# Performance work log

Measured on AMD Instinct MI355X. Metric: run time of the kernel, lower is better.

Reference implementation:

```python
import jax, jax.numpy as jnp
import numpy as np

B, L = 16, 512
H_RNN = 300
EMB, POSD, POSTD = 300, 30, 30
IN_DIM = EMB + POSD + POSTD  # 360
HEADS, MEM = 8, 300
DM = 2 * MEM                 # 600
DK = DM // HEADS             # 75
VOCAB, NPOS, NPOST = 30000, 50, 120
ALPHA, BETA = 0.8, 0.9
N_ASP = 3


def _lstm_dir(x, w_ih, w_hh, b_ih, b_hh, reverse):
    # x: [B,L,D] -> [B,L,H]; PyTorch gate order i,f,g,o
    xs = jnp.swapaxes(x, 0, 1)
    if reverse:
        xs = xs[::-1]
    pre = xs @ w_ih.T + (b_ih + b_hh)  # [L,B,4H]
    Bn = x.shape[0]
    H = w_hh.shape[1]

    def step(carry, p):
        h, c = carry
        g = p + h @ w_hh.T
        i, f, gg, o = jnp.split(g, 4, axis=-1)
        c = jax.nn.sigmoid(f) * c + jax.nn.sigmoid(i) * jnp.tanh(gg)
        h = jax.nn.sigmoid(o) * jnp.tanh(c)
        return (h, c), h

    init = (jnp.zeros((Bn, H), x.dtype), jnp.zeros((Bn, H), x.dtype))
    _, hs = jax.lax.scan(step, init, pre)
    if reverse:
        hs = hs[::-1]
    return jnp.swapaxes(hs, 0, 1)


def _forward(tok, pos, post, asp_mask, adj_reshape, emb_w, pos_w, post_w,
             w_ih_f, w_hh_f, b_ih_f, b_hh_f, w_ih_b, w_hh_b, b_ih_b, b_hh_b,
             wq, bq, wk, bk, wd, bd, weight_m, bias_m,
             wa0, ba0, wa1, ba1, ws0, bs0, ws1, bs1, affine1, affine2):
    Bn, Ln = tok.shape
    embs = jnp.concatenate([emb_w[tok], pos_w[pos], post_w[post]], -1)  # [B,L,360]
    hf = _lstm_dir(embs, w_ih_f, w_hh_f, b_ih_f, b_hh_f, False)
    hb = _lstm_dir(embs, w_ih_b, w_hh_b, b_ih_b, b_hh_b, True)
    gcn_inputs = jnp.concatenate([hf, hb], -1)  # [B,L,600]
    tok_mask = tok != 0
    aspect_outs = gcn_inputs * asp_mask[:, :, None]

    q = (gcn_inputs @ wq.T + bq).reshape(Bn, Ln, HEADS, DK).transpose(0, 2, 1, 3)
    k = (gcn_inputs @ wk.T + bk).reshape(Bn, Ln, HEADS, DK).transpose(0, 2, 1, 3)
    aspd = aspect_outs @ wd.T + bd  # [B,L,DK], shared across heads
    t = jnp.einsum('bld,hde->bhle', aspd, weight_m)
    asps = jnp.tanh(jnp.einsum('bhle,bhme->bhlm', t, k) + bias_m[0])  # [B,h,L,L]

    # fusion branch: vectorized equivalent of the ragged row/col scatter-average.
    # Original loop: for each aspect idx (ascending), row idx <- avg vec, then col idx <- avg vec.
    avg = asps.sum(-2) / Ln  # [B,h,L]
    amask = asp_mask > 0
    r = jnp.arange(Ln)[:, None]
    c = jnp.arange(Ln)[None, :]
    rA = amask[:, None, :, None]
    cA = amask[:, None, None, :]
    col_wins = cA & (~rA | (c > r))
    aspect_scores = jnp.where(col_wins, avg[:, :, :, None],
                              jnp.where(rA, avg[:, :, None, :], asps))

    scores = jnp.einsum('bhld,bhmd->bhlm', q, k) / np.float32(np.sqrt(DK))
    scores = jnp.where(tok_mask[:, None, None, :], scores, -1e9)
    s_attn = jax.nn.softmax(scores, -1)

    asavg = aspect_scores.mean(1)  # [B,L,L]
    adj_s = s_attn.mean(1)
    eye = jnp.eye(Ln, dtype=adj_s.dtype)
    adj_s = (adj_s * (1.0 - eye) + eye) * tok_mask[:, :, None].astype(adj_s.dtype)

    adj_r = jnp.where(asavg > BETA, 1.0, jnp.exp(ALPHA * adj_reshape))
    adj_ag = adj_r * asavg

    denom_s = adj_s.sum(2, keepdims=True) + 1.0
    denom_ag = adj_ag.sum(2, keepdims=True) + 1.0
    out_ag = out_s = gcn_inputs
    for wa_, ba_, ws_, bs_ in ((wa0, ba0, ws0, bs0), (wa1, ba1, ws1, bs1)):
        g_ag = jax.nn.relu(((adj_ag @ out_ag) @ wa_.T + ba_) / denom_ag)
        g_s = jax.nn.relu(((adj_s @ out_s) @ ws_.T + bs_) / denom_s)
        A1 = jax.nn.softmax(jnp.einsum('bld,de,bme->blm', g_ag, affine1, g_s), -1)
        A2 = jax.nn.softmax(jnp.einsum('bld,de,bme->blm', g_s, affine2, g_ag), -1)
        out_ag, out_s = A1 @ g_s, A2 @ g_ag
    return jnp.concatenate([out_ag, out_s], -1)  # [B,L,600]


def setup_inputs():
    key = jax.random.key(0)
    ks = jax.random.split(key, 40)

    def nrm(i, shape):
        return jax.random.normal(ks[i], shape, jnp.float32) * 0.02

    tok = jax.random.randint(ks[0], (B, L), 1, VOCAB, jnp.int32)
    pos = jax.random.randint(ks[1], (B, L), 0, NPOS, jnp.int32)
    post = jax.random.randint(ks[2], (B, L), 0, NPOST, jnp.int32)
    asp_mask = jnp.zeros((B, L), jnp.float32).at[:, 3:3 + N_ASP].set(1.0)
    l = jnp.full((B,), L, jnp.int32)
    adj_reshape = jax.random.uniform(ks[3], (B, L, L), jnp.float32)
    return dict(
        tok=tok, pos=pos, post=post, asp_mask=asp_mask, l=l, adj_reshape=adj_reshape,
        emb_w=nrm(4, (VOCAB, EMB)), pos_w=nrm(5, (NPOS, POSD)), post_w=nrm(6, (NPOST, POSTD)),
        w_ih_f=nrm(7, (4 * H_RNN, IN_DIM)), w_hh_f=nrm(8, (4 * H_RNN, H_RNN)),
        b_ih_f=nrm(9, (4 * H_RNN,)), b_hh_f=nrm(10, (4 * H_RNN,)),
        w_ih_b=nrm(11, (4 * H_RNN, IN_DIM)), w_hh_b=nrm(12, (4 * H_RNN, H_RNN)),
        b_ih_b=nrm(13, (4 * H_RNN,)), b_hh_b=nrm(14, (4 * H_RNN,)),
        wq=nrm(15, (DM, DM)), bq=nrm(16, (DM,)), wk=nrm(17, (DM, DM)), bk=nrm(18, (DM,)),
        wd=nrm(19, (DK, DM)), bd=nrm(20, (DK,)),
        weight_m=nrm(21, (HEADS, DK, DK)), bias_m=nrm(22, (1,)),
        wa0=nrm(23, (MEM, DM)), ba0=nrm(24, (MEM,)), wa1=nrm(25, (MEM, MEM)), ba1=nrm(26, (MEM,)),
        ws0=nrm(27, (MEM, DM)), bs0=nrm(28, (MEM,)), ws1=nrm(29, (MEM, MEM)), bs1=nrm(30, (MEM,)),
        affine1=nrm(31, (MEM, MEM)), affine2=nrm(32, (MEM, MEM)))


def reference(tok, pos, post, asp_mask, l, adj_reshape, emb_w, pos_w, post_w,
              w_ih_f, w_hh_f, b_ih_f, b_hh_f, w_ih_b, w_hh_b, b_ih_b, b_hh_b,
              wq, bq, wk, bk, wd, bd, weight_m, bias_m,
              wa0, ba0, wa1, ba1, ws0, bs0, ws1, bs1, affine1, affine2):
    # l is all-maxlen by construction (no padding); pack/pad is identity.
    return _forward(tok, pos, post, asp_mask, adj_reshape, emb_w, pos_w, post_w,
                    w_ih_f, w_hh_f, b_ih_f, b_hh_f, w_ih_b, w_hh_b, b_ih_b, b_hh_b,
                    wq, bq, wk, bk, wd, bd, weight_m, bias_m,
                    wa0, ba0, wa1, ba1, ws0, bs0, ws1, bs1, affine1, affine2)
```

## Files before the change

kernel.cpp:

```cpp
#include <hip/hip_runtime.h>
#include <hip/hip_bf16.h>

typedef __hip_bfloat16 bf16;
typedef __attribute__((ext_vector_type(4))) short short4v;
typedef __attribute__((ext_vector_type(8))) short short8v;
typedef __attribute__((ext_vector_type(4))) float f32x4;
typedef unsigned long long u64;

#define B_   16
#define L_   512
#define HR   300
#define DM_  600
#define DK_  75
#define MAXA 8
#define NCH  38

__global__ __launch_bounds__(256) void k_embed(
    const int* __restrict__ tok, const int* __restrict__ pos, const int* __restrict__ post,
    const float* __restrict__ emb_w, const float* __restrict__ pos_w, const float* __restrict__ post_w,
    float* __restrict__ embs)
{
  int idx = blockIdx.x * 256 + threadIdx.x;
  if (idx >= L_ * B_ * 360) return;
  int d = idx % 360;
  int seq = idx / 360;
  int b = seq & 15, t = seq >> 4;
  int si = b * L_ + t;
  float v;
  if (d < 300)       v = emb_w[(long)tok[si] * 300 + d];
  else if (d < 330)  v = pos_w[pos[si] * 30 + (d - 300)];
  else               v = post_w[post[si] * 30 + (d - 330)];
  embs[idx] = v;
}

__global__ __launch_bounds__(256) void k_stage(
    const float* __restrict__ wq, const float* __restrict__ wk,
    const float* __restrict__ bq, const float* __restrict__ bk,
    const float* __restrict__ wihf, const float* __restrict__ wihb,
    const float* __restrict__ aff1, const float* __restrict__ aff2,
    const float* __restrict__ ws0, const float* __restrict__ wa0,
    const float* __restrict__ ws1, const float* __restrict__ wa1,
    const float* __restrict__ bs0, const float* __restrict__ ba0,
    const float* __restrict__ bs1, const float* __restrict__ ba1,
    float* __restrict__ wqk, float* __restrict__ bqk,
    float* __restrict__ wih, float* __restrict__ aff,
    float* __restrict__ wsa, float* __restrict__ bsa)
{
  int i = blockIdx.x * 256 + threadIdx.x;
  if (i < 360000) wqk[i] = wq[i];
  else if (i < 720000) wqk[i] = wk[i - 360000];
  else if (i < 720600) bqk[i - 720000] = bq[i - 720000];
  else if (i < 721200) bqk[i - 720000] = bk[i - 720600];
  else if (i < 1153200) wih[i - 721200] = wihf[i - 721200];
  else if (i < 1585200) wih[i - 721200] = wihb[i - 1153200];
  else if (i < 1675200) aff[i - 1585200] = aff1[i - 1585200];
  else if (i < 1765200) aff[i - 1585200] = aff2[i - 1675200];
  else if (i < 1945200) wsa[i - 1765200] = ws0[i - 1765200];
  else if (i < 2125200) wsa[i - 1765200] = wa0[i - 1945200];
  else if (i < 2215200) wsa[i - 1765200] = ws1[i - 2125200];
  else if (i < 2305200) wsa[i - 1765200] = wa1[i - 2215200];
  else if (i < 2305500) bsa[i - 2305200] = bs0[i - 2305200];
  else if (i < 2305800) bsa[i - 2305200] = ba0[i - 2305500];
  else if (i < 2306100) bsa[i - 2305200] = bs1[i - 2305800];
  else if (i < 2306400) bsa[i - 2305200] = ba1[i - 2306100];
}

__device__ inline short2 splitf(float x) {
  unsigned u = __float_as_uint(x);
  unsigned hb = u & 0xffff0000u;
  float r = x - __uint_as_float(hb);
  unsigned lb = __float_as_uint(r);
  short2 out;
  out.x = (short)(hb >> 16);
  out.y = (short)(lb >> 16);
  return out;
}

__device__ inline short8v ld_frag(const short* p) {
  short4v a = *reinterpret_cast<const short4v*>(p);
  short4v b = *reinterpret_cast<const short4v*>(p + 16);
  short8v r;
  r[0]=a[0]; r[1]=a[1]; r[2]=a[2]; r[3]=a[3];
  r[4]=b[0]; r[5]=b[1]; r[6]=b[2]; r[7]=b[3];
  return r;
}

#define LDA_ 36

template<bool NT>
__global__ __launch_bounds__(256) void k_mgemm(
    const float* __restrict__ A, int lda, long sA1, long sA2,
    const float* __restrict__ Bm, int ldb, long sB1, long sB2,
    float* __restrict__ C, bf16* __restrict__ Cbf, int ldc, long sC1, long sC2,
    const float* __restrict__ bias, long sBias,
    const float* __restrict__ rowdiv,
    float alpha, int relu, int M, int N, int K, int nb2)
{
  __shared__ short Ah[128 * LDA_], Al[128 * LDA_], Bh[64 * LDA_], Bl[64 * LDA_];
  const int tid = threadIdx.x;
  const int w = tid >> 6, l = tid & 63;
  const int z = blockIdx.z;
  const int b1 = z / nb2, b2 = z - b1 * nb2;
  const float* Ab = A + b1 * sA1 + b2 * sA2;
  const float* Bb = Bm + b1 * sB1 + b2 * sB2;
  const int row0 = blockIdx.y * 128, col0 = blockIdx.x * 64;

  f32x4 acc[2][4];
#pragma unroll
  for (int f = 0; f < 2; ++f)
#pragma unroll
    for (int c = 0; c < 4; ++c) acc[f][c] = (f32x4){0.f, 0.f, 0.f, 0.f};

  const int lrow = l & 15, lk = (l >> 4) * 4;

  for (int k0 = 0; k0 < K; k0 += 32) {
#pragma unroll
    for (int j = 0; j < 4; ++j) {
      int slot = j * 256 + tid;
      int r = slot >> 3, kq = slot & 7;
      int gr = row0 + r, gk = k0 + kq * 4;
      float v[4] = {0.f, 0.f, 0.f, 0.f};
      if (gr < M) {
        if (gk + 3 < K) {
          float4 t = *reinterpret_cast<const float4*>(Ab + (long)gr * lda + gk);
          v[0] = t.x; v[1] = t.y; v[2] = t.z; v[3] = t.w;
        } else {
#pragma unroll
          for (int q = 0; q < 4; ++q) if (gk + q < K) v[q] = Ab[(long)gr * lda + gk + q];
        }
      }
      short4v hv, lv;
#pragma unroll
      for (int q = 0; q < 4; ++q) {
        short2 t2 = splitf(v[q]);
        hv[q] = t2.x; lv[q] = t2.y;
      }
      *reinterpret_cast<short4v*>(&Ah[r * LDA_ + kq * 4]) = hv;
      *reinterpret_cast<short4v*>(&Al[r * LDA_ + kq * 4]) = lv;
    }
    if (NT) {
#pragma unroll
      for (int j = 0; j < 2; ++j) {
        int slot = j * 256 + tid;
        int r = slot >> 3, kq = slot & 7;
        int gc = col0 + r, gk = k0 + kq * 4;
        float v[4] = {0.f, 0.f, 0.f, 0.f};
        if (gc < N) {
          if (gk + 3 < K) {
            float4 t = *reinterpret_cast<const float4*>(Bb + (long)gc * ldb + gk);
            v[0] = t.x; v[1] = t.y; v[2] = t.z; v[3] = t.w;
          } else {
#pragma unroll
            for (int q = 0; q < 4; ++q) if (gk + q < K) v[q] = Bb[(long)gc * ldb + gk + q];
          }
        }
        short4v hv, lv;
#pragma unroll
        for (int q = 0; q < 4; ++q) {
          short2 t2 = splitf(v[q]);
          hv[q] = t2.x; lv[q] = t2.y;
        }
        *reinterpret_cast<short4v*>(&Bh[r * LDA_ + kq * 4]) = hv;
        *reinterpret_cast<short4v*>(&Bl[r * LDA_ + kq * 4]) = lv;
      }
    } else {
#pragma unroll
      for (int j = 0; j < 2; ++j) {
        int slot = j * 256 + tid;
        int kk = slot >> 4, nq = slot & 15;
        int gk = k0 + kk, gn = col0 + nq * 4;
        float v[4] = {0.f, 0.f, 0.f, 0.f};
        if (gk < K) {
          if (gn + 3 < N) {
            float4 t = *reinterpret_cast<const float4*>(Bb + (long)gk * ldb + gn);
            v[0] = t.x; v[1] = t.y; v[2] = t.z; v[3] = t.w;
          } else {
#pragma unroll
            for (int q = 0; q < 4; ++q) if (gn + q < N) v[q] = Bb[(long)gk * ldb + gn + q];
          }
        }
#pragma unroll
        for (int q = 0; q < 4; ++q) {
          short2 t2 = splitf(v[q]);
          Bh[(nq * 4 + q) * LDA_ + kk] = t2.x;
          Bl[(nq * 4 + q) * LDA_ + kk] = t2.y;
        }
      }
    }
    __syncthreads();

    short8v ah[2], al[2];
#pragma unroll
    for (int f = 0; f < 2; ++f) {
      int ar = w * 32 + f * 16 + lrow;
      ah[f] = ld_frag(&Ah[ar * LDA_ + lk]);
      al[f] = ld_frag(&Al[ar * LDA_ + lk]);
    }
#pragma unroll
    for (int c = 0; c < 4; ++c) {
      short8v bh = ld_frag(&Bh[(c * 16 + lrow) * LDA_ + lk]);
      short8v bl = ld_frag(&Bl[(c * 16 + lrow) * LDA_ + lk]);
#pragma unroll
      for (int f = 0; f < 2; ++f) {
        acc[f][c] = __builtin_amdgcn_mfma_f32_16x16x32_bf16(ah[f], bh, acc[f][c], 0, 0, 0);
        acc[f][c] = __builtin_amdgcn_mfma_f32_16x16x32_bf16(ah[f], bl, acc[f][c], 0, 0, 0);
        acc[f][c] = __builtin_amdgcn_mfma_f32_16x16x32_bf16(al[f], bh, acc[f][c], 0, 0, 0);
      }
    }
    __syncthreads();
  }

  float* Cb = C ? C + b1 * sC1 + b2 * sC2 : (float*)0;
  bf16*  Cf = Cbf ? Cbf + b1 * sC1 + b2 * sC2 : (bf16*)0;
#pragma unroll
  for (int f = 0; f < 2; ++f)
#pragma unroll
  for (int c = 0; c < 4; ++c) {
    int cc = col0 + c * 16 + lrow;
    if (cc >= N) continue;
#pragma unroll
    for (int reg = 0; reg < 4; ++reg) {
      int r = row0 + w * 32 + f * 16 + (l >> 4) * 4 + reg;
      if (r >= M) continue;
      float v = acc[f][c][reg] * alpha;
      if (bias) v += bias[b1 * sBias + cc];
      if (rowdiv) v /= rowdiv[(long)z * M + r];
      if (relu) v = fmaxf(v, 0.f);
      if (Cf) Cf[(long)r * ldc + cc] = __float2bfloat16(v);
      else    Cb[(long)r * ldc + cc] = v;
    }
  }
}

__global__ __launch_bounds__(512, 1) void k_lstm(
    const float* __restrict__ preT_f, const float* __restrict__ preT_b,
    const float* __restrict__ whh_f, const float* __restrict__ whh_b,
    const float* __restrict__ bih_f, const float* __restrict__ bhh_f,
    const float* __restrict__ bih_b, const float* __restrict__ bhh_b,
    float* __restrict__ gcn, u64* __restrict__ hg)
{
  const int tid = threadIdx.x;
  const int dir = blockIdx.x / NCH;
  const int blk = blockIdx.x - dir * NCH;
  const int u0 = blk * 8;
  const int uc = min(8, HR - u0);
  const float* pre = dir ? preT_b : preT_f;
  const float* whh = dir ? whh_b : whh_f;
  const float* bih = dir ? bih_b : bih_f;
  const float* bhh = dir ? bhh_b : bhh_f;
  u64* hgd = hg + dir * 2400;

  __shared__ float4 h5[1200];
  __shared__ float part[32 * 545 + 64];
  __shared__ float g_lds[512];
  float* h5f = reinterpret_cast<float*>(h5);

  const int kc = tid >> 4;
  const int rq = tid & 15;
  const int kl = (kc < 12) ? 10 : 9;
  const int k0 = kc * 9 + min(kc, 12);

  float wreg[2][10];
#pragma unroll
  for (int i = 0; i < 2; ++i) {
    int lr = rq * 2 + i;
    int gate = lr >> 3, unit = lr & 7;
    bool valid = unit < uc;
    int growc = gate * HR + u0 + min(unit, uc - 1);
#pragma unroll
    for (int kk = 0; kk < 10; ++kk) {
      int k = min(k0 + kk, 299);
      float wv = whh[(long)growc * HR + k];
      wreg[i][kk] = (valid && kk < kl) ? wv : 0.f;
    }
  }

  const int lr0 = tid >> 4;
  const int b0 = tid & 15;
  const int gate0 = lr0 >> 3, unit0 = lr0 & 7;
  const int grow0 = gate0 * HR + u0 + min(unit0, uc - 1);
  const float breg = bih[grow0] + bhh[grow0];
  const float* prebase = pre + (long)grow0 * 8192;

  const int au = tid >> 3, abp = tid & 7;
  float c_reg0 = 0.f, c_reg1 = 0.f;

  const int own_lo = u0 * 8, own_hi = (u0 + uc) * 8;

#pragma unroll 1
  for (int s = 0; s < L_; ++s) {
    const int tf = dir ? (L_ - 1 - s) : s;

    float p0 = prebase[tf * 16 + b0];

    if (s > 0) {
      u64* srcb = hgd + (s & 1) * 4800;
      const u64 tag = (u64)s;
      u64 vals[5];
      int idxs[5];
#pragma unroll
      for (int j = 0; j < 5; ++j) {
        int idx = tid + j * 512;
        bool act = (idx < 2400) && (idx < own_lo || idx >= own_hi);
        idxs[j] = act ? idx : -1;
        vals[j] = act ? __hip_atomic_load(&srcb[idx], __ATOMIC_RELAXED, __HIP_MEMORY_SCOPE_AGENT)
                      : (tag << 32);
      }
      for (;;) {
        bool ok = true;
#pragma unroll
        for (int j = 0; j < 5; ++j)
          if ((vals[j] >> 32) != tag) ok = false;
        if (ok) break;
#pragma unroll
        for (int j = 0; j < 5; ++j)
          if ((vals[j] >> 32) != tag)
            vals[j] = __hip_atomic_load(&srcb[idxs[j]], __ATOMIC_RELAXED, __HIP_MEMORY_SCOPE_AGENT);
      }
#pragma unroll
      for (int j = 0; j < 5; ++j) {
        int idx = idxs[j];
        if (idx >= 0) {
          unsigned lo = (unsigned)(vals[j] & 0xffffffffu);
          unsigned short be = (unsigned short)(lo & 0xffffu);
          unsigned short bo = (unsigned short)(lo >> 16);
          bf16 he = *reinterpret_cast<bf16*>(&be);
          bf16 ho = *reinterpret_cast<bf16*>(&bo);
          int u = idx >> 3, bp = idx & 7;
          h5f[u * 16 + bp * 2]     = __bfloat162float(he);
          h5f[u * 16 + bp * 2 + 1] = __bfloat162float(ho);
        }
      }
    }
    __syncthreads();

    if (s > 0) {
      float4 acc[2][4];
#pragma unroll
      for (int i = 0; i < 2; ++i)
#pragma unroll
        for (int q = 0; q < 4; ++q) acc[i][q] = make_float4(0.f, 0.f, 0.f, 0.f);
#pragma unroll
      for (int kk = 0; kk < 10; ++kk) {
        if (kk < kl) {
          int k = k0 + kk;
          float4 hb0 = h5[k * 4 + 0];
          float4 hb1 = h5[k * 4 + 1];
          float4 hb2 = h5[k * 4 + 2];
          float4 hb3 = h5[k * 4 + 3];
#pragma unroll
          for (int i = 0; i < 2; ++i) {
            float w = wreg[i][kk];
            acc[i][0].x = fmaf(w, hb0.x, acc[i][0].x); acc[i][0].y = fmaf(w, hb0.y, acc[i][0].y);
            acc[i][0].z = fmaf(w, hb0.z, acc[i][0].z); acc[i][0].w = fmaf(w, hb0.w, acc[i][0].w);
            acc[i][1].x = fmaf(w, hb1.x, acc[i][1].x); acc[i][1].y = fmaf(w, hb1.y, acc[i][1].y);
            acc[i][1].z = fmaf(w, hb1.z, acc[i][1].z); acc[i][1].w = fmaf(w, hb1.w, acc[i][1].w);
            acc[i][2].x = fmaf(w, hb2.x, acc[i][2].x); acc[i][2].y = fmaf(w, hb2.y, acc[i][2].y);
            acc[i][2].z = fmaf(w, hb2.z, acc[i][2].z); acc[i][2].w = fmaf(w, hb2.w, acc[i][2].w);
            acc[i][3].x = fmaf(w, hb3.x, acc[i][3].x); acc[i][3].y = fmaf(w, hb3.y, acc[i][3].y);
            acc[i][3].z = fmaf(w, hb3.z, acc[i][3].z); acc[i][3].w = fmaf(w, hb3.w, acc[i][3].w);
          }
        }
      }
#pragma unroll
      for (int i = 0; i < 2; ++i) {
        int lr = rq * 2 + i;
        float* pb = part + kc * 545 + lr * 17;
#pragma unroll
        for (int q = 0; q < 4; ++q) {
          pb[q * 4 + 0] = acc[i][q].x; pb[q * 4 + 1] = acc[i][q].y;
          pb[q * 4 + 2] = acc[i][q].z; pb[q * 4 + 3] = acc[i][q].w;
        }
      }
    }
    __syncthreads();

    float g0 = p0 + breg;
    if (s > 0) {
      const float* pb = part + lr0 * 17 + b0;
#pragma unroll
      for (int q = 0; q < 32; ++q) g0 += pb[q * 545];
    }
    g_lds[tid] = g0;
    __syncthreads();

    if (tid < 64 && au < uc) {
      int be = abp * 2, bo = abp * 2 + 1;
      float gi0 = g_lds[(0 * 8 + au) * 16 + be];
      float gf0 = g_lds[(1 * 8 + au) * 16 + be];
      float gg0 = g_lds[(2 * 8 + au) * 16 + be];
      float go0 = g_lds[(3 * 8 + au) * 16 + be];
      float gi1 = g_lds[(0 * 8 + au) * 16 + bo];
      float gf1 = g_lds[(1 * 8 + au) * 16 + bo];
      float gg1 = g_lds[(2 * 8 + au) * 16 + bo];
      float go1 = g_lds[(3 * 8 + au) * 16 + bo];
      float si0 = 1.f / (1.f + __expf(-gi0));
      float sf0 = 1.f / (1.f + __expf(-gf0));
      float so0 = 1.f / (1.f + __expf(-go0));
      float tg0 = tanhf(gg0);
      float si1 = 1.f / (1.f + __expf(-gi1));
      float sf1 = 1.f / (1.f + __expf(-gf1));
      float so1 = 1.f / (1.f + __expf(-go1));
      float tg1 = tanhf(gg1);
      c_reg0 = sf0 * c_reg0 + si0 * tg0;
      c_reg1 = sf1 * c_reg1 + si1 * tg1;
      float h0 = so0 * tanhf(c_reg0);
      float h1 = so1 * tanhf(c_reg1);
      h5f[(u0 + au) * 16 + be] = h0;
      h5f[(u0 + au) * 16 + bo] = h1;
      bf16 hbe = __float2bfloat16(h0);
      bf16 hbo = __float2bfloat16(h1);
      unsigned bitse = *reinterpret_cast<unsigned short*>(&hbe);
      unsigned bitso = *reinterpret_cast<unsigned short*>(&hbo);
      u64 val = ((u64)(s + 1) << 32) | ((u64)bitso << 16) | (u64)bitse;
      __hip_atomic_store(&hgd[((s + 1) & 1) * 4800 + (u0 + au) * 8 + abp], val,
                         __ATOMIC_RELAXED, __HIP_MEMORY_SCOPE_AGENT);
      gcn[((long)be * L_ + tf) * DM_ + dir * HR + u0 + au] = h0;
      gcn[((long)bo * L_ + tf) * DM_ + dir * HR + u0 + au] = h1;
    }
  }
}

__global__ void k_asplist(const float* __restrict__ asp_mask, int* __restrict__ apos, int* __restrict__ acnt)
{
  int b = threadIdx.x;
  if (b >= B_) return;
  int c = 0;
  for (int l = 0; l < L_; ++l)
    if (asp_mask[b * L_ + l] > 0.f) { if (c < MAXA) apos[b * MAXA + c] = l; ++c; }
  acnt[b] = (c < MAXA) ? c : MAXA;
}

__global__ void k_t0(const float* __restrict__ bd, const float* __restrict__ wm, float* __restrict__ t0)
{
  int i = blockIdx.x * 256 + threadIdx.x;
  if (i >= 8 * DK_) return;
  int h = i / DK_, e = i % DK_;
  float s = 0.f;
  for (int d = 0; d < DK_; ++d) s += bd[d] * wm[(h * DK_ + d) * DK_ + e];
  t0[i] = s;
}

__global__ void k_aspd(const float* __restrict__ gcn, const float* __restrict__ asp_mask,
                       const int* __restrict__ apos, const int* __restrict__ acnt,
                       const float* __restrict__ wd, const float* __restrict__ bd, float* __restrict__ aspd)
{
  int i = blockIdx.x * 256 + threadIdx.x;
  if (i >= B_ * MAXA * DK_) return;
  int d = i % DK_;
  int ba = i / DK_;
  int a = ba % MAXA, b = ba / MAXA;
  if (a >= acnt[b]) { aspd[i] = 0.f; return; }
  int p = apos[b * MAXA + a];
  float mv = asp_mask[b * L_ + p];
  const float* row = gcn + ((long)b * L_ + p) * DM_;
  float s = 0.f;
  for (int k = 0; k < DM_; ++k) s += row[k] * wd[d * DM_ + k];
  aspd[i] = s * mv + bd[d];
}

__global__ void k_tasp(const float* __restrict__ aspd, const int* __restrict__ acnt,
                       const float* __restrict__ wm, float* __restrict__ tasp)
{
  int i = blockIdx.x * 256 + threadIdx.x;
  if (i >= B_ * 8 * MAXA * DK_) return;
  int e = i % DK_;
  int t3 = i / DK_;
  int a = t3 % MAXA;
  int t4 = t3 / MAXA;
  int h = t4 % 8, b = t4 / 8;
  if (a >= acnt[b]) { tasp[i] = 0.f; return; }
  const float* ar = aspd + (b * MAXA + a) * DK_;
  float s = 0.f;
  for (int d = 0; d < DK_; ++d) s += ar[d] * wm[(h * DK_ + d) * DK_ + e];
  tasp[i] = s;
}

__global__ void k_avg(const float* __restrict__ k_lin, const float* __restrict__ t0,
                      const float* __restrict__ tasp, const int* __restrict__ acnt,
                      const float* __restrict__ bias_m, float* __restrict__ s0, float* __restrict__ avg)
{
  int i = blockIdx.x * 256 + threadIdx.x;
  if (i >= B_ * 8 * L_) return;
  int m = i % L_;
  int bh = i / L_;
  int h = bh % 8, b = bh / 8;
  const float* kr = k_lin + ((long)b * L_ + m) * DM_ + h * DK_;
  float bm = bias_m[0];
  const float* t0r = t0 + h * DK_;
  float d0 = 0.f;
  for (int e = 0; e < DK_; ++e) d0 += t0r[e] * kr[e];
  float sv = tanhf(d0 + bm);
  int cnt = acnt[b];
  float acc = (float)(L_ - cnt) * sv;
  for (int a = 0; a < cnt; ++a) {
    const float* tr = tasp + (((b * 8 + h) * MAXA) + a) * DK_;
    float dd = 0.f;
    for (int e = 0; e < DK_; ++e) dd += tr[e] * kr[e];
    acc += tanhf(dd + bm);
  }
  s0[i] = sv;
  avg[i] = acc * (1.f / (float)L_);
}

__global__ void k_bar(const float* __restrict__ s0, const float* __restrict__ avg,
                      float* __restrict__ s0bar, float* __restrict__ avbar)
{
  int i = blockIdx.x * 256 + threadIdx.x;
  if (i >= B_ * L_) return;
  int m = i % L_, b = i / L_;
  float sa = 0.f, aa = 0.f;
  for (int h = 0; h < 8; ++h) { sa += s0[(b * 8 + h) * L_ + m]; aa += avg[(b * 8 + h) * L_ + m]; }
  s0bar[i] = sa * 0.125f;
  avbar[i] = aa * 0.125f;
}

__global__ __launch_bounds__(256) void k_adjag(
    const float* __restrict__ asp_mask, const float* __restrict__ adjr,
    const float* __restrict__ s0bar, const float* __restrict__ avbar,
    float* __restrict__ adjag, float* __restrict__ denag)
{
  int bl = blockIdx.x;
  int b = bl >> 9, l = bl & 511;
  bool rA = asp_mask[b * L_ + l] > 0.f;
  float avl = avbar[b * L_ + l];
  float lsum = 0.f;
  for (int q = 0; q < 2; ++q) {
    int m = threadIdx.x + q * 256;
    bool cA = asp_mask[b * L_ + m] > 0.f;
    float asv;
    if (cA && (!rA || m > l)) asv = avl;
    else if (rA)              asv = avbar[b * L_ + m];
    else                      asv = s0bar[b * L_ + m];
    float r = (asv > 0.9f) ? 1.f : __expf(0.8f * adjr[((long)b * L_ + l) * L_ + m]);
    float v = r * asv;
    adjag[((long)b * L_ + l) * L_ + m] = v;
    lsum += v;
  }
  __shared__ float red[256];
  red[threadIdx.x] = lsum;
  __syncthreads();
  for (int st = 128; st > 0; st >>= 1) {
    if (threadIdx.x < st) red[threadIdx.x] += red[threadIdx.x + st];
    __syncthreads();
  }
  if (threadIdx.x == 0) denag[bl] = red[0] + 1.f;
}

__global__ __launch_bounds__(256) void k_adjs2(
    const bf16* __restrict__ sc, const int* __restrict__ tok,
    float* __restrict__ adjs, float* __restrict__ dens)
{
  int bl = blockIdx.x;
  int b = bl >> 9, l = bl & 511;
  int tid = threadIdx.x;
  __shared__ float srow[8][512];
  __shared__ float stats[16];
  __shared__ float red[256];

  int t0v = tok[b * L_ + tid], t1v = tok[b * L_ + tid + 256];
#pragma unroll
  for (int h = 0; h < 8; ++h) {
    const bf16* p = sc + ((long)((b * 8 + h) * L_) + l) * L_;
    float v0 = __bfloat162float(p[tid]);
    float v1 = __bfloat162float(p[tid + 256]);
    srow[h][tid]       = (t0v != 0) ? v0 : -1e9f;
    srow[h][tid + 256] = (t1v != 0) ? v1 : -1e9f;
  }
  __syncthreads();

  int wv = tid >> 6, lane = tid & 63;
#pragma unroll
  for (int hh = 0; hh < 2; ++hh) {
    int h = wv * 2 + hh;
    float vv[8];
#pragma unroll
    for (int i = 0; i < 8; ++i) vv[i] = srow[h][lane + i * 64];
    float m = vv[0];
#pragma unroll
    for (int i = 1; i < 8; ++i) m = fmaxf(m, vv[i]);
    for (int off = 32; off > 0; off >>= 1) m = fmaxf(m, __shfl_xor(m, off));
    float s = 0.f;
#pragma unroll
    for (int i = 0; i < 8; ++i) s += __expf(vv[i] - m);
    for (int off = 32; off > 0; off >>= 1) s += __shfl_xor(s, off);
    if (lane == 0) { stats[h] = m; stats[8 + h] = 1.f / s; }
  }
  __syncthreads();

  float acc0 = 0.f, acc1 = 0.f;
#pragma unroll
  for (int h = 0; h < 8; ++h) {
    float m = stats[h], inv = stats[8 + h];
    acc0 += __expf(srow[h][tid] - m) * inv;
    acc1 += __expf(srow[h][tid + 256] - m) * inv;
  }
  float rmask = (tok[b * L_ + l] != 0) ? 1.f : 0.f;
  float lsum = 0.f;
  {
    int m = tid;
    float v = acc0 * 0.125f;
    v = (m == l) ? 1.f : v;
    v *= rmask;
    adjs[(long)bl * L_ + m] = v;
    lsum += v;
  }
  {
    int m = tid + 256;
    float v = acc1 * 0.125f;
    v = (m == l) ? 1.f : v;
    v *= rmask;
    adjs[(long)bl * L_ + m] = v;
    lsum += v;
  }
  red[tid] = lsum;
  __syncthreads();
  for (int st = 128; st > 0; st >>= 1) {
    if (tid < st) red[tid] += red[tid + st];
    __syncthreads();
  }
  if (tid == 0) dens[bl] = red[0] + 1.f;
}

__global__ __launch_bounds__(256) void k_softmax(float* __restrict__ X)
{
  long row = blockIdx.x;
  float* p = X + row * L_;
  int tid = threadIdx.x;
  float a = p[tid], b = p[tid + 256];
  __shared__ float red[256];
  red[tid] = fmaxf(a, b);
  __syncthreads();
  for (int st = 128; st > 0; st >>= 1) {
    if (tid < st) red[tid] = fmaxf(red[tid], red[tid + st]);
    __syncthreads();
  }
  float mxv = red[0];
  __syncthreads();
  float ea = __expf(a - mxv), eb = __expf(b - mxv);
  red[tid] = ea + eb;
  __syncthreads();
  for (int st = 128; st > 0; st >>= 1) {
    if (tid < st) red[tid] += red[tid + st];
    __syncthreads();
  }
  float inv = 1.f / red[0];
  p[tid] = ea * inv;
  p[tid + 256] = eb * inv;
}

static void gemm(hipStream_t st, bool nt,
                 const float* A, int lda, long sA1, long sA2,
                 const float* Bm, int ldb, long sB1, long sB2,
                 float* C, bf16* Cbf, int ldc, long sC1, long sC2,
                 const float* bias, long sBias, const float* rowdiv,
                 float alpha, int relu, int M, int N, int K, int nb1, int nb2)
{
  dim3 g((N + 63) / 64, (M + 127) / 128, nb1 * nb2);
  if (nt)
    k_mgemm<true><<<g, 256, 0, st>>>(A, lda, sA1, sA2, Bm, ldb, sB1, sB2, C, Cbf, ldc, sC1, sC2,
                                     bias, sBias, rowdiv, alpha, relu, M, N, K, nb2);
  else
    k_mgemm<false><<<g, 256, 0, st>>>(A, lda, sA1, sA2, Bm, ldb, sB1, sB2, C, Cbf, ldc, sC1, sC2,
                                      bias, sBias, rowdiv, alpha, relu, M, N, K, nb2);
}

extern "C" void kernel_launch(void* const* d_in, const int* in_sizes, int n_in,
                              void* d_out, int out_size, void* d_ws, size_t ws_size,
                              hipStream_t stream)
{
  const int*   tok     = (const int*)d_in[0];
  const int*   pos     = (const int*)d_in[1];
  const int*   post    = (const int*)d_in[2];
  const float* asp_mask= (const float*)d_in[3];
  const float* adjr    = (const float*)d_in[5];
  const float* emb_w   = (const float*)d_in[6];
  const float* pos_w   = (const float*)d_in[7];
  const float* post_w  = (const float*)d_in[8];
  const float* w_ih_f  = (const float*)d_in[9];
  const float* w_hh_f  = (const float*)d_in[10];
  const float* b_ih_f  = (const float*)d_in[11];
  const float* b_hh_f  = (const float*)d_in[12];
  const float* w_ih_b  = (const float*)d_in[13];
  const float* w_hh_b  = (const float*)d_in[14];
  const float* b_ih_b  = (const float*)d_in[15];
  const float* b_hh_b  = (const float*)d_in[16];
  const float* wq      = (const float*)d_in[17];
  const float* bq      = (const float*)d_in[18];
  const float* wk      = (const float*)d_in[19];
  const float* bk      = (const float*)d_in[20];
  const float* wd      = (const float*)d_in[21];
  const float* bd      = (const float*)d_in[22];
  const float* wm      = (const float*)d_in[23];
  const float* bias_m  = (const float*)d_in[24];
  const float* wa0     = (const float*)d_in[25];
  const float* ba0     = (const float*)d_in[26];
  const float* wa1     = (const float*)d_in[27];
  const float* ba1     = (const float*)d_in[28];
  const float* ws0     = (const float*)d_in[29];
  const float* bs0     = (const float*)d_in[30];
  const float* ws1     = (const float*)d_in[31];
  const float* bs1     = (const float*)d_in[32];
  const float* aff1    = (const float*)d_in[33];
  const float* aff2    = (const float*)d_in[34];
  float* out = (float*)d_out;
  float* W = (float*)d_ws;

  size_t off = 0;
  auto alloc = [&](size_t n) { size_t o = off; off += (n + 63) & ~(size_t)63; return o; };
  size_t o_gcn   = alloc((size_t)8192 * DM_);
  size_t o_q     = alloc((size_t)8192 * DM_);
  size_t o_k     = alloc((size_t)8192 * DM_);
  size_t o_adjs  = alloc((size_t)B_ * L_ * L_);
  size_t o_adjag = alloc((size_t)B_ * L_ * L_);
  size_t o_dens  = alloc(8192);
  size_t o_denag = alloc(8192);
  size_t o_t0    = alloc(600);
  size_t o_apos  = alloc(B_ * MAXA);
  size_t o_acnt  = alloc(64);
  size_t o_aspd  = alloc(B_ * MAXA * DK_);
  size_t o_tasp  = alloc(B_ * 8 * MAXA * DK_);
  size_t o_s0    = alloc(B_ * 8 * L_);
  size_t o_avg   = alloc(B_ * 8 * L_);
  size_t o_s0bar = alloc(B_ * L_);
  size_t o_avbar = alloc(B_ * L_);
  size_t o_hg    = alloc(2 * 2 * 4800);
  size_t o_wqk   = alloc(720000);
  size_t o_bqk   = alloc(1200);
  size_t o_wih   = alloc(864000);
  size_t o_aff   = alloc(180000);
  size_t o_wsa   = alloc(540000);
  size_t o_bsa   = alloc(1200);
  size_t o_oag1  = alloc((size_t)8192 * 300);
  size_t o_os1   = alloc((size_t)8192 * 300);
  size_t o_big   = alloc(23134300);
  size_t o_embs = o_big;
  size_t o_pref = o_big + 2949120;
  size_t o_preb = o_pref + 9830400;
  size_t o_sc   = o_big;
  size_t o_tmp  = o_big;
  size_t o_gag  = o_big + 4915200;
  size_t o_gs   = o_gag + 2457600;
  size_t o_h1   = o_gs  + 2457600;
  size_t o_a1m  = o_h1  + 4915200;
  size_t o_a2m  = o_a1m + 4194304;

  if (ws_size < off * sizeof(float)) {
    (void)hipMemsetAsync(d_out, 0x7F, (size_t)out_size * sizeof(float), stream);
    return;
  }

  k_stage<<<(2306400 + 255) / 256, 256, 0, stream>>>(
      wq, wk, bq, bk, w_ih_f, w_ih_b, aff1, aff2,
      ws0, wa0, ws1, wa1, bs0, ba0, bs1, ba1,
      W + o_wqk, W + o_bqk, W + o_wih, W + o_aff, W + o_wsa, W + o_bsa);

  k_embed<<<(L_ * B_ * 360 + 255) / 256, 256, 0, stream>>>(tok, pos, post, emb_w, pos_w, post_w, W + o_embs);

  gemm(stream, true, W + o_wih, 360, 432000, 0, W + o_embs, 360, 0, 0,
       W + o_pref, nullptr, 8192, 9830400, 0, nullptr, 0, nullptr, 1.f, 0, 1200, 8192, 360, 2, 1);

  k_lstm<<<2 * NCH, 512, 0, stream>>>(W + o_pref, W + o_preb, w_hh_f, w_hh_b,
                                      b_ih_f, b_hh_f, b_ih_b, b_hh_b,
                                      W + o_gcn, (u64*)(W + o_hg));

  gemm(stream, true, W + o_gcn, DM_, 0, 0, W + o_wqk, DM_, 360000, 0,
       W + o_q, nullptr, DM_, (long)(o_k - o_q), 0, W + o_bqk, 600, nullptr,
       1.f, 0, 8192, DM_, DM_, 2, 1);

  k_asplist<<<1, 64, 0, stream>>>(asp_mask, (int*)(W + o_apos), (int*)(W + o_acnt));
  k_t0<<<(600 + 255) / 256, 256, 0, stream>>>(bd, wm, W + o_t0);
  k_aspd<<<(B_ * MAXA * DK_ + 255) / 256, 256, 0, stream>>>(W + o_gcn, asp_mask,
      (const int*)(W + o_apos), (const int*)(W + o_acnt), wd, bd, W + o_aspd);
  k_tasp<<<(B_ * 8 * MAXA * DK_ + 255) / 256, 256, 0, stream>>>(W + o_aspd,
      (const int*)(W + o_acnt), wm, W + o_tasp);
  k_avg<<<(B_ * 8 * L_ + 255) / 256, 256, 0, stream>>>(W + o_k, W + o_t0, W + o_tasp,
      (const int*)(W + o_acnt), bias_m, W + o_s0, W + o_avg);
  k_bar<<<(B_ * L_ + 255) / 256, 256, 0, stream>>>(W + o_s0, W + o_avg, W + o_s0bar, W + o_avbar);

  gemm(stream, true, W + o_q, DM_, (long)L_ * DM_, DK_, W + o_k, DM_, (long)L_ * DM_, DK_,
       nullptr, (bf16*)(W + o_sc), L_, (long)8 * L_ * L_, (long)L_ * L_,
       nullptr, 0, nullptr, 0.1154700538f, 0, L_, L_, DK_, B_, 8);
  k_adjs2<<<B_ * L_, 256, 0, stream>>>((const bf16*)(W + o_sc), tok, W + o_adjs, W + o_dens);
  k_adjag<<<B_ * L_, 256, 0, stream>>>(asp_mask, adjr, W + o_s0bar, W + o_avbar,
                                       W + o_adjag, W + o_denag);

  const float* inBase;
  long inStride;
  const long tmpStride = (long)o_tmp - (long)o_a1m;
  int D = DM_;
  for (int layer = 0; layer < 2; ++layer) {
    if (layer == 0) { inBase = W + o_gcn; inStride = 0; }
    else            { inBase = W + o_os1; inStride = (long)o_oag1 - (long)o_os1; }
    gemm(stream, false,
         W + o_adjs, L_, (long)o_adjag - (long)o_adjs, (long)L_ * L_,
         inBase, D, inStride, (long)L_ * D,
         W + o_a1m, nullptr, D, tmpStride, (long)L_ * D,
         nullptr, 0, nullptr, 1.f, 0, L_, D, L_, 2, B_);
    gemm(stream, true,
         W + o_a1m, D, tmpStride, 0,
         W + o_wsa + (layer ? 360000 : 0), D, (layer ? 90000 : 180000), 0,
         W + o_gs, nullptr, 300, (long)o_gag - (long)o_gs, 0,
         W + o_bsa + (layer ? 600 : 0), 300, W + o_dens,
         1.f, 1, 8192, 300, D, 2, 1);
    gemm(stream, false, W + o_gag, 300, (long)(o_gs - o_gag), 0, W + o_aff, 300, 90000, 0,
         W + o_h1, nullptr, 300, 2457600, 0, nullptr, 0, nullptr, 1.f, 0, 8192, 300, 300, 2, 1);
    gemm(stream, true, W + o_h1, 300, 2457600, (long)L_ * 300,
         W + o_gs, 300, (long)o_gag - (long)o_gs, (long)L_ * 300,
         W + o_a1m, nullptr, L_, 4194304, (long)L_ * L_,
         nullptr, 0, nullptr, 1.f, 0, L_, L_, 300, 2, B_);
    k_softmax<<<2 * B_ * L_, 256, 0, stream>>>(W + o_a1m);
    float* dstC; int ldcO; long sC1o, sC2o;
    if (layer == 0) { dstC = W + o_oag1; ldcO = 300; sC1o = (long)(o_os1 - o_oag1); sC2o = (long)L_ * 300; }
    else            { dstC = out;        ldcO = 600; sC1o = 300;                    sC2o = (long)L_ * 600; }
    gemm(stream, false, W + o_a1m, L_, 4194304, (long)L_ * L_,
         W + o_gs, 300, (long)o_gag - (long)o_gs, (long)L_ * 300,
         dstC, nullptr, ldcO, sC1o, sC2o,
         nullptr, 0, nullptr, 1.f, 0, L_, 300, L_, 2, B_);
    D = 300;
  }
}
```

Before: 2.779 ms.

## Split LSTM recurrence across 75 blocks per direction with 4 units each

```diff
diff --git a/kernel.cpp b/kernel.cpp
--- a/kernel.cpp
+++ b/kernel.cpp
@@ -13,7 +13,7 @@
 #define DM_  600
 #define DK_  75
 #define MAXA 8
-#define NCH  38
+#define NCH  75
 
 __global__ __launch_bounds__(256) void k_embed(
     const int* __restrict__ tok, const int* __restrict__ pos, const int* __restrict__ post,
@@ -242,8 +242,7 @@
   const int tid = threadIdx.x;
   const int dir = blockIdx.x / NCH;
   const int blk = blockIdx.x - dir * NCH;
-  const int u0 = blk * 8;
-  const int uc = min(8, HR - u0);
+  const int u0 = blk * 4;
   const float* pre = dir ? preT_b : preT_f;
   const float* whh = dir ? whh_b : whh_f;
   const float* bih = dir ? bih_b : bih_f;
@@ -251,8 +250,8 @@
   u64* hgd = hg + dir * 2400;
 
   __shared__ float4 h5[1200];
-  __shared__ float part[32 * 545 + 64];
-  __shared__ float g_lds[512];
+  __shared__ float part[32 * 273 + 16];
+  __shared__ float g_lds[256];
   float* h5f = reinterpret_cast<float*>(h5);
 
   const int kc = tid >> 4;
@@ -260,32 +259,30 @@
   const int kl = (kc < 12) ? 10 : 9;
   const int k0 = kc * 9 + min(kc, 12);
 
-  float wreg[2][10];
-#pragma unroll
-  for (int i = 0; i < 2; ++i) {
-    int lr = rq * 2 + i;
-    int gate = lr >> 3, unit = lr & 7;
-    bool valid = unit < uc;
-    int growc = gate * HR + u0 + min(unit, uc - 1);
+  float wreg[10];
+  {
+    int gate = rq >> 2, unit = rq & 3;
+    int grow = gate * HR + u0 + unit;
 #pragma unroll
     for (int kk = 0; kk < 10; ++kk) {
       int k = min(k0 + kk, 299);
-      float wv = whh[(long)growc * HR + k];
-      wreg[i][kk] = (valid && kk < kl) ? wv : 0.f;
-    }
-  }
-
-  const int lr0 = tid >> 4;
-  const int b0 = tid & 15;
-  const int gate0 = lr0 >> 3, unit0 = lr0 & 7;
-  const int grow0 = gate0 * HR + u0 + min(unit0, uc - 1);
+      float wv = whh[(long)grow * HR + k];
+      wreg[kk] = (kk < kl) ? wv : 0.f;
+    }
+  }
+
+  const int e0 = tid >> 1;
+  const int half = tid & 1;
+  const int lr0 = e0 >> 4, b0 = e0 & 15;
+  const int gate0 = lr0 >> 2, unit0 = lr0 & 3;
+  const int grow0 = gate0 * HR + u0 + unit0;
   const float breg = bih[grow0] + bhh[grow0];
   const float* prebase = pre + (long)grow0 * 8192;
 
   const int au = tid >> 3, abp = tid & 7;
   float c_reg0 = 0.f, c_reg1 = 0.f;
 
-  const int own_lo = u0 * 8, own_hi = (u0 + uc) * 8;
+  const int own_lo = u0 * 8, own_hi = (u0 + 4) * 8;
 
 #pragma unroll 1
   for (int s = 0; s < L_; ++s) {
@@ -335,11 +332,9 @@
     __syncthreads();
 
     if (s > 0) {
-      float4 acc[2][4];
-#pragma unroll
-      for (int i = 0; i < 2; ++i)
-#pragma unroll
-        for (int q = 0; q < 4; ++q) acc[i][q] = make_float4(0.f, 0.f, 0.f, 0.f);
+      float4 acc[4];
+#pragma unroll
+      for (int q = 0; q < 4; ++q) acc[q] = make_float4(0.f, 0.f, 0.f, 0.f);
 #pragma unroll
       for (int kk = 0; kk < 10; ++kk) {
         if (kk < kl) {
@@ -348,52 +343,46 @@
           float4 hb1 = h5[k * 4 + 1];
           float4 hb2 = h5[k * 4 + 2];
           float4 hb3 = h5[k * 4 + 3];
-#pragma unroll
-          for (int i = 0; i < 2; ++i) {
-            float w = wreg[i][kk];
-            acc[i][0].x = fmaf(w, hb0.x, acc[i][0].x); acc[i][0].y = fmaf(w, hb0.y, acc[i][0].y);
-            acc[i][0].z = fmaf(w, hb0.z, acc[i][0].z); acc[i][0].w = fmaf(w, hb0.w, acc[i][0].w);
-            acc[i][1].x = fmaf(w, hb1.x, acc[i][1].x); acc[i][1].y = fmaf(w, hb1.y, acc[i][1].y);
-            acc[i][1].z = fmaf(w, hb1.z, acc[i][1].z); acc[i][1].w = fmaf(w, hb1.w, acc[i][1].w);
-            acc[i][2].x = fmaf(w, hb2.x, acc[i][2].x); acc[i][2].y = fmaf(w, hb2.y, acc[i][2].y);
-            acc[i][2].z = fmaf(w, hb2.z, acc[i][2].z); acc[i][2].w = fmaf(w, hb2.w, acc[i][2].w);
-            acc[i][3].x = fmaf(w, hb3.x, acc[i][3].x); acc[i][3].y = fmaf(w, hb3.y, acc[i][3].y);
-            acc[i][3].z = fmaf(w, hb3.z, acc[i][3].z); acc[i][3].w = fmaf(w, hb3.w, acc[i][3].w);
-          }
+          float w = wreg[kk];
+          acc[0].x = fmaf(w, hb0.x, acc[0].x); acc[0].y = fmaf(w, hb0.y, acc[0].y);
+          acc[0].z = fmaf(w, hb0.z, acc[0].z); acc[0].w = fmaf(w, hb0.w, acc[0].w);
+          acc[1].x = fmaf(w, hb1.x, acc[1].x); acc[1].y = fmaf(w, hb1.y, acc[1].y);
+          acc[1].z = fmaf(w, hb1.z, acc[1].z); acc[1].w = fmaf(w, hb1.w, acc[1].w);
+          acc[2].x = fmaf(w, hb2.x, acc[2].x); acc[2].y = fmaf(w, hb2.y, acc[2].y);
+          acc[2].z = fmaf(w, hb2.z, acc[2].z); acc[2].w = fmaf(w, hb2.w, acc[2].w);
+          acc[3].x = fmaf(w, hb3.x, acc[3].x); acc[3].y = fmaf(w, hb3.y, acc[3].y);
+          acc[3].w = fmaf(w, hb3.w, acc[3].w); acc[3].z = fmaf(w, hb3.z, acc[3].z);
         }
       }
-#pragma unroll
-      for (int i = 0; i < 2; ++i) {
-        int lr = rq * 2 + i;
-        float* pb = part + kc * 545 + lr * 17;
-#pragma unroll
-        for (int q = 0; q < 4; ++q) {
-          pb[q * 4 + 0] = acc[i][q].x; pb[q * 4 + 1] = acc[i][q].y;
-          pb[q * 4 + 2] = acc[i][q].z; pb[q * 4 + 3] = acc[i][q].w;
-        }
+      float* pb = part + kc * 273 + rq * 17;
+#pragma unroll
+      for (int q = 0; q < 4; ++q) {
+        pb[q * 4 + 0] = acc[q].x; pb[q * 4 + 1] = acc[q].y;
+        pb[q * 4 + 2] = acc[q].z; pb[q * 4 + 3] = acc[q].w;
       }
     }
     __syncthreads();
 
-    float g0 = p0 + breg;
+    float sum = 0.f;
     if (s > 0) {
-      const float* pb = part + lr0 * 17 + b0;
-#pragma unroll
-      for (int q = 0; q < 32; ++q) g0 += pb[q * 545];
-    }
-    g_lds[tid] = g0;
+      const float* pb = part + half * 16 * 273 + lr0 * 17 + b0;
+#pragma unroll
+      for (int q = 0; q < 16; ++q) sum += pb[q * 273];
+    }
+    float other = __shfl_xor(sum, 1);
+    if (half == 0) g_lds[e0] = p0 + breg + sum + other;
     __syncthreads();
 
-    if (tid < 64 && au < uc) {
+    if (tid < 32) {
       int be = abp * 2, bo = abp * 2 + 1;
-      float gi0 = g_lds[(0 * 8 + au) * 16 + be];
-      float gf0 = g_lds[(1 * 8 + au) * 16 + be];
-      float gg0 = g_lds[(2 * 8 + au) * 16 + be];
-      float go0 = g_lds[(3 * 8 + au) * 16 + be];
-      float gi1 = g_lds[(0 * 8 + au) * 16 + bo];
-      float gf1 = g_lds[(1 * 8 + au) * 16 + bo];
-      float gg1 = g_lds[(2 * 8 + au) * 16 + bo];
-      float go1 = g_lds[(3 * 8 + au) * 16 + bo];
+      float gi0 = g_lds[(0 * 4 + au) * 16 + be];
+      float gf0 = g_lds[(1 * 4 + au) * 16 + be];
+      float gg0 = g_lds[(2 * 4 + au) * 16 + be];
+      float go0 = g_lds[(3 * 4 + au) * 16 + be];
+      float gi1 = g_lds[(0 * 4 + au) * 16 + bo];
+      float gf1 = g_lds[(1 * 4 + au) * 16 + bo];
+      float gg1 = g_lds[(2 * 4 + au) * 16 + bo];
+      float go1 = g_lds[(3 * 4 + au) * 16 + bo];
       float si0 = 1.f / (1.f + __expf(-gi0));
       float sf0 = 1.f / (1.f + __expf(-gf0));
       float so0 = 1.f / (1.f + __expf(-go0));
```

After: 2.515 ms. -9.5%, faster.
